# Performance work log

Hardware: AMD Instinct MI355X
Metric: run time of the kernel (lower is better)

Reference implementation:

```python
import jax, jax.numpy as jnp
import numpy as np


def setup_inputs() -> dict:
    key = jax.random.key(0)
    k1, k2 = jax.random.split(key)
    n, k = 131072, 512
    inp = jax.random.normal(k1, (n, k), dtype=jnp.float32)
    target = jax.random.uniform(k2, (n, k), dtype=jnp.float32)
    return {"input": inp, "target": target}


def reference(input, target):
    # Soft cross entropy: loss_i = -sum_y target[i,y] * log_softmax(input)[i,y]
    # (weight=None). Single fused log_softmax replaces the original k-fold loop.
    logp = jax.nn.log_softmax(input, axis=-1)  # [n, k]
    cum_losses = -jnp.sum(target * logp, axis=-1)  # [n]
    # reduction == 'elementwise_mean'
    return jnp.mean(cum_losses)
```

## Files before the change

kernel.cpp:

```cpp
#include <hip/hip_runtime.h>
#include <hip/hip_bf16.h>


#define K_COLS 512

__global__ __launch_bounds__(256, 4)
void sce_kernel(const float* __restrict__ inp, const float* __restrict__ tgt,
                float* __restrict__ out, int n, float inv_n) {
    const int lane = threadIdx.x & 63;
    const int half = lane >> 5;
    const int j    = lane & 31;
    const int wave = threadIdx.x >> 6;
    const int gwave = blockIdx.x * 4 + wave;
    const int total_waves = gridDim.x * 4;

    float acc = 0.0f;

    for (int base = gwave * 2; base < n; base += total_waves * 2) {
        const int row = base + half;
        const float4* ip = (const float4*)(inp + (size_t)row * K_COLS);
        const float4* tp = (const float4*)(tgt + (size_t)row * K_COLS);
        float4 x0 = ip[j];
        float4 x1 = ip[j + 32];
        float4 x2 = ip[j + 64];
        float4 x3 = ip[j + 96];
        float4 t0 = tp[j];
        float4 t1 = tp[j + 32];
        float4 t2 = tp[j + 64];
        float4 t3 = tp[j + 96];

        float es = __expf(x0.x) + __expf(x0.y) + __expf(x0.z) + __expf(x0.w)
                 + __expf(x1.x) + __expf(x1.y) + __expf(x1.z) + __expf(x1.w)
                 + __expf(x2.x) + __expf(x2.y) + __expf(x2.z) + __expf(x2.w)
                 + __expf(x3.x) + __expf(x3.y) + __expf(x3.z) + __expf(x3.w);
        float ts = (t0.x + t0.y + t0.z + t0.w) + (t1.x + t1.y + t1.z + t1.w)
                 + (t2.x + t2.y + t2.z + t2.w) + (t3.x + t3.y + t3.z + t3.w);
        float tx = 0.0f;
        tx = fmaf(t0.x, x0.x, tx); tx = fmaf(t0.y, x0.y, tx);
        tx = fmaf(t0.z, x0.z, tx); tx = fmaf(t0.w, x0.w, tx);
        tx = fmaf(t1.x, x1.x, tx); tx = fmaf(t1.y, x1.y, tx);
        tx = fmaf(t1.z, x1.z, tx); tx = fmaf(t1.w, x1.w, tx);
        tx = fmaf(t2.x, x2.x, tx); tx = fmaf(t2.y, x2.y, tx);
        tx = fmaf(t2.z, x2.z, tx); tx = fmaf(t2.w, x2.w, tx);
        tx = fmaf(t3.x, x3.x, tx); tx = fmaf(t3.y, x3.y, tx);
        tx = fmaf(t3.z, x3.z, tx); tx = fmaf(t3.w, x3.w, tx);

        #pragma unroll
        for (int off = 16; off > 0; off >>= 1) {
            es += __shfl_xor(es, off, 64);
            ts += __shfl_xor(ts, off, 64);
            tx += __shfl_xor(tx, off, 64);
        }

        acc = fmaf(__logf(es), ts, acc - tx);
    }

    acc += __shfl_xor(acc, 32, 64);
    __shared__ float smem[4];
    if (lane == 0) smem[wave] = acc;
    __syncthreads();
    if (threadIdx.x == 0) {
        float b = (smem[0] + smem[1]) + (smem[2] + smem[3]);
        atomicAdd(out, b * inv_n);
    }
}

extern "C" void kernel_launch(void* const* d_in, const int* in_sizes, int n_in,
                              void* d_out, int out_size, void* d_ws, size_t ws_size,
                              hipStream_t stream) {
    const float* inp = (const float*)d_in[0];
    const float* tgt = (const float*)d_in[1];
    float* out = (float*)d_out;
    const int n = in_sizes[0] / K_COLS;

    hipMemsetAsync(out, 0, sizeof(float), stream);

    const int blocks = 8192;
    sce_kernel<<<blocks, 256, 0, stream>>>(inp, tgt, out, n, 1.0f / (float)n);
}
```

Before: 514.4 us.

## Batch eight row-pairs per wave and replace atomic with two-pass reduction

Each wave now handles a fixed block of 16 rows, issuing all loads for eight row-pairs before any cross-lane shuffles so more memory requests are in flight. The grid-stride loop is gone, and the grid is sized to cover n exactly. The global atomicAdd and memset are replaced by per-block partials in workspace plus a single-block final reduction kernel. This adds a second launch and raises register pressure from holding eight pairs of float4 data.

```diff
diff --git a/kernel.cpp b/kernel.cpp
--- a/kernel.cpp
+++ b/kernel.cpp
@@ -3,66 +3,83 @@
 
 
 #define K_COLS 512
+#define PAIRS 8
 
 __global__ __launch_bounds__(256, 4)
-void sce_kernel(const float* __restrict__ inp, const float* __restrict__ tgt,
-                float* __restrict__ out, int n, float inv_n) {
+void sce_partial(const float* __restrict__ inp, const float* __restrict__ tgt,
+                 float* __restrict__ ws, int n) {
     const int lane = threadIdx.x & 63;
     const int half = lane >> 5;
     const int j    = lane & 31;
     const int wave = threadIdx.x >> 6;
     const int gwave = blockIdx.x * 4 + wave;
-    const int total_waves = gridDim.x * 4;
+
+    float es[PAIRS], ts[PAIRS], tx[PAIRS];
+    const int base = gwave * (2 * PAIRS);
+
+    #pragma unroll
+    for (int p = 0; p < PAIRS; ++p) {
+        const int row0 = base + 2 * p + half;
+        const int row  = (row0 < n) ? row0 : 0;
+        const float4* ip = (const float4*)(inp + (size_t)row * K_COLS);
+        const float4* tp = (const float4*)(tgt + (size_t)row * K_COLS);
+        float4 x0 = ip[j];       float4 x1 = ip[j + 32];
+        float4 x2 = ip[j + 64];  float4 x3 = ip[j + 96];
+        float4 t0 = tp[j];       float4 t1 = tp[j + 32];
+        float4 t2 = tp[j + 64];  float4 t3 = tp[j + 96];
+
+        es[p] = __expf(x0.x) + __expf(x0.y) + __expf(x0.z) + __expf(x0.w)
+              + __expf(x1.x) + __expf(x1.y) + __expf(x1.z) + __expf(x1.w)
+              + __expf(x2.x) + __expf(x2.y) + __expf(x2.z) + __expf(x2.w)
+              + __expf(x3.x) + __expf(x3.y) + __expf(x3.z) + __expf(x3.w);
+        ts[p] = (t0.x + t0.y + t0.z + t0.w) + (t1.x + t1.y + t1.z + t1.w)
+              + (t2.x + t2.y + t2.z + t2.w) + (t3.x + t3.y + t3.z + t3.w);
+        float v = 0.0f;
+        v = fmaf(t0.x, x0.x, v); v = fmaf(t0.y, x0.y, v);
+        v = fmaf(t0.z, x0.z, v); v = fmaf(t0.w, x0.w, v);
+        v = fmaf(t1.x, x1.x, v); v = fmaf(t1.y, x1.y, v);
+        v = fmaf(t1.z, x1.z, v); v = fmaf(t1.w, x1.w, v);
+        v = fmaf(t2.x, x2.x, v); v = fmaf(t2.y, x2.y, v);
+        v = fmaf(t2.z, x2.z, v); v = fmaf(t2.w, x2.w, v);
+        v = fmaf(t3.x, x3.x, v); v = fmaf(t3.y, x3.y, v);
+        v = fmaf(t3.z, x3.z, v); v = fmaf(t3.w, x3.w, v);
+        tx[p] = v;
+    }
 
     float acc = 0.0f;
-
-    for (int base = gwave * 2; base < n; base += total_waves * 2) {
-        const int row = base + half;
-        const float4* ip = (const float4*)(inp + (size_t)row * K_COLS);
-        const float4* tp = (const float4*)(tgt + (size_t)row * K_COLS);
-        float4 x0 = ip[j];
-        float4 x1 = ip[j + 32];
-        float4 x2 = ip[j + 64];
-        float4 x3 = ip[j + 96];
-        float4 t0 = tp[j];
-        float4 t1 = tp[j + 32];
-        float4 t2 = tp[j + 64];
-        float4 t3 = tp[j + 96];
-
-        float es = __expf(x0.x) + __expf(x0.y) + __expf(x0.z) + __expf(x0.w)
-                 + __expf(x1.x) + __expf(x1.y) + __expf(x1.z) + __expf(x1.w)
-                 + __expf(x2.x) + __expf(x2.y) + __expf(x2.z) + __expf(x2.w)
-                 + __expf(x3.x) + __expf(x3.y) + __expf(x3.z) + __expf(x3.w);
-        float ts = (t0.x + t0.y + t0.z + t0.w) + (t1.x + t1.y + t1.z + t1.w)
-                 + (t2.x + t2.y + t2.z + t2.w) + (t3.x + t3.y + t3.z + t3.w);
-        float tx = 0.0f;
-        tx = fmaf(t0.x, x0.x, tx); tx = fmaf(t0.y, x0.y, tx);
-        tx = fmaf(t0.z, x0.z, tx); tx = fmaf(t0.w, x0.w, tx);
-        tx = fmaf(t1.x, x1.x, tx); tx = fmaf(t1.y, x1.y, tx);
-        tx = fmaf(t1.z, x1.z, tx); tx = fmaf(t1.w, x1.w, tx);
-        tx = fmaf(t2.x, x2.x, tx); tx = fmaf(t2.y, x2.y, tx);
-        tx = fmaf(t2.z, x2.z, tx); tx = fmaf(t2.w, x2.w, tx);
-        tx = fmaf(t3.x, x3.x, tx); tx = fmaf(t3.y, x3.y, tx);
-        tx = fmaf(t3.z, x3.z, tx); tx = fmaf(t3.w, x3.w, tx);
-
+    #pragma unroll
+    for (int p = 0; p < PAIRS; ++p) {
+        float e = es[p], t = ts[p], x = tx[p];
         #pragma unroll
         for (int off = 16; off > 0; off >>= 1) {
-            es += __shfl_xor(es, off, 64);
-            ts += __shfl_xor(ts, off, 64);
-            tx += __shfl_xor(tx, off, 64);
+            e += __shfl_xor(e, off, 64);
+            t += __shfl_xor(t, off, 64);
+            x += __shfl_xor(x, off, 64);
         }
+        const float valid = (base + 2 * p + half < n) ? 1.0f : 0.0f;
+        acc += valid * (__logf(e) * t - x);
+    }
+    acc += __shfl_xor(acc, 32, 64);
 
-        acc = fmaf(__logf(es), ts, acc - tx);
-    }
-
-    acc += __shfl_xor(acc, 32, 64);
     __shared__ float smem[4];
     if (lane == 0) smem[wave] = acc;
     __syncthreads();
-    if (threadIdx.x == 0) {
-        float b = (smem[0] + smem[1]) + (smem[2] + smem[3]);
-        atomicAdd(out, b * inv_n);
-    }
+    if (threadIdx.x == 0)
+        ws[blockIdx.x] = (smem[0] + smem[1]) + (smem[2] + smem[3]);
+}
+
+__global__ __launch_bounds__(256)
+void sce_reduce(const float* __restrict__ ws, float* __restrict__ out,
+                int nblocks, float inv_n) {
+    float s = 0.0f;
+    for (int i = threadIdx.x; i < nblocks; i += 256) s += ws[i];
+    #pragma unroll
+    for (int off = 32; off > 0; off >>= 1) s += __shfl_xor(s, off, 64);
+    __shared__ float sm[4];
+    if ((threadIdx.x & 63) == 0) sm[threadIdx.x >> 6] = s;
+    __syncthreads();
+    if (threadIdx.x == 0)
+        out[0] = ((sm[0] + sm[1]) + (sm[2] + sm[3])) * inv_n;
 }
 
 extern "C" void kernel_launch(void* const* d_in, const int* in_sizes, int n_in,
@@ -71,10 +88,12 @@
     const float* inp = (const float*)d_in[0];
     const float* tgt = (const float*)d_in[1];
     float* out = (float*)d_out;
+    float* ws  = (float*)d_ws;
     const int n = in_sizes[0] / K_COLS;
 
-    hipMemsetAsync(out, 0, sizeof(float), stream);
+    const int rows_per_block = 4 * 2 * PAIRS;
+    const int blocks = (n + rows_per_block - 1) / rows_per_block;
 
-    const int blocks = 8192;
-    sce_kernel<<<blocks, 256, 0, stream>>>(inp, tgt, out, n, 1.0f / (float)n);
+    sce_partial<<<blocks, 256, 0, stream>>>(inp, tgt, ws, n);
+    sce_reduce<<<1, 256, 0, stream>>>(ws, out, blocks, 1.0f / (float)n);
 }
```

New measurement: 497.8 us. 3.2% less time.
